# Kernel tuning notes

Measured on AMD Instinct MI355X. Metric: run time of the kernel, lower is better.

## Reference

```python
import jax, jax.numpy as jnp
import numpy as np

B, S, K, N, G = 4, 16, 8192, 8192, 128
NUM_GROUPS = K // G

def setup_inputs() -> dict:
    key = jax.random.key(0)
    k1, k2, k3, k4, k5 = jax.random.split(key, 5)
    x = jax.random.normal(k1, (B, S, K), dtype=jnp.float32)
    qweight = jax.random.randint(k2, (K, N), -128, 128, dtype=jnp.int32)
    # small positive scales like real quantizers produce
    scales = jax.random.uniform(k3, (NUM_GROUPS, N), dtype=jnp.float32) * 0.01 + 1e-4
    zeros = jax.random.uniform(k4, (NUM_GROUPS, N), dtype=jnp.float32) * 2.0 - 1.0
    bias = jax.random.normal(k5, (N,), dtype=jnp.float32)
    return {"x": x, "qweight": qweight, "scales": scales, "zeros": zeros,
            "bias": bias, "group_size": G}

def reference(x, qweight, scales, zeros, bias, group_size):
    # Expand per-group scale/zero along K: [num_groups, N] -> [K, N]
    Kdim = qweight.shape[0]
    if scales.shape[0] == 1:
        scale_exp = jnp.broadcast_to(scales, (Kdim, scales.shape[1]))
        zero_exp = jnp.broadcast_to(zeros, (Kdim, zeros.shape[1]))
    else:
        scale_exp = jnp.repeat(scales, group_size, axis=0)[:Kdim]
        zero_exp = jnp.repeat(zeros, group_size, axis=0)[:Kdim]
    # Dequantize: W[k, n] = (q - zero) * scale
    weight_fp = (qweight.astype(x.dtype) - zero_exp) * scale_exp  # [K, N]
    out = jnp.einsum('bsk,kn->bsn', x, weight_fp) + bias
    return out
```

## Files before the change

### kernel.cpp

```cpp
#include <hip/hip_runtime.h>

typedef __attribute__((ext_vector_type(8))) short short8;
typedef __attribute__((ext_vector_type(8))) unsigned short ushort8;
typedef __attribute__((ext_vector_type(4))) unsigned short ushort4v;
typedef __attribute__((ext_vector_type(4))) int int4v;
typedef __attribute__((ext_vector_type(4))) float f32x4;

#define Mdim 64
#define Kdim 8192
#define Ndim 8192
#define GRP 128
#define NGRP 64
#define KSPLIT 4
#define NG2 (NGRP / KSPLIT)
#define BN 128

#define SWZ(row, kk) ((row)*128 + ((kk) ^ (8*((((row) >> 3) ^ (row)) & 7))))

__device__ __forceinline__ unsigned short f2bf(float f) {
    unsigned int u = __builtin_bit_cast(unsigned int, f);
    u += 0x7FFFu + ((u >> 16) & 1u);
    return (unsigned short)(u >> 16);
}
__device__ __forceinline__ float bf2f(unsigned short h) {
    unsigned int u = ((unsigned int)h) << 16;
    return __builtin_bit_cast(float, u);
}

__global__ void prep_kernel(const float* __restrict__ x,
                            unsigned short* __restrict__ xh,
                            unsigned short* __restrict__ xl,
                            float* __restrict__ xsum) {
    const int tid = threadIdx.x;
    const int u = blockIdx.x * 8 + (tid >> 5);
    const int g = u & (NGRP - 1);
    const int m = u >> 6;
    const int lane = tid & 31;
    const int k = g * GRP + lane * 4;
    f32x4 v = *(const f32x4*)(x + (size_t)m * Kdim + k);
    ushort4v hv, lv;
    float s = 0.f;
#pragma unroll
    for (int i = 0; i < 4; ++i) {
        unsigned short h = f2bf(v[i]);
        hv[i] = h;
        lv[i] = f2bf(v[i] - bf2f(h));
        s += v[i];
    }
    *(ushort4v*)(xh + (size_t)m * Kdim + k) = hv;
    *(ushort4v*)(xl + (size_t)m * Kdim + k) = lv;
#pragma unroll
    for (int off = 16; off > 0; off >>= 1) s += __shfl_down(s, off, 32);
    if (lane == 0) xsum[g * Mdim + m] = s;
}

__global__ void init_kernel(const float* __restrict__ bias,
                            float* __restrict__ out) {
    const size_t e = ((size_t)blockIdx.x * 256 + threadIdx.x) * 4;
    const int n = (int)(e & (Ndim - 1));
    *(f32x4*)(out + e) = *(const f32x4*)(bias + n);
}

__launch_bounds__(512, 2)
__global__ void qlin_kernel(const unsigned short* __restrict__ xh,
                            const unsigned short* __restrict__ xl,
                            const int* __restrict__ qw,
                            const float* __restrict__ scales,
                            const float* __restrict__ zeros,
                            const float* __restrict__ xsum,
                            float* __restrict__ out) {
    __shared__ unsigned short lq[2][128 * 128];
    __shared__ unsigned short lxh[2][64 * 128];
    __shared__ unsigned short lxl[2][64 * 128];
    __shared__ float ls[NG2][128];
    __shared__ float lz[NG2][128];
    __shared__ float lxs[NG2][64];

    const int tid = threadIdx.x;
    const int kh = blockIdx.x & (KSPLIT - 1);
    const int n0 = (blockIdx.x >> 2) * BN;
    const int g0 = kh * NG2;

    const int w = tid >> 6;
    const int l = tid & 63;
    const int lcol = l & 15;
    const int lhi = l >> 4;
    const int mt = (w >> 2) * 32;
    const int ns = (w & 3) * 32;

    const int qc = tid & 31;
    const int qr = tid >> 5;
    const int xc = tid & 15;
    const int xm = tid >> 4;

    const int c0 = n0 + ns + lcol;
    const int c1 = c0 + 16;

    int4v qv[8];
    ushort8 xga, xgb, xgc, xgd;

    auto LOADX = [&](int g) {
        const size_t kb = (size_t)g * GRP + xc * 8;
        xga = *(const ushort8*)(xh + (size_t)xm * Kdim + kb);
        xgb = *(const ushort8*)(xh + (size_t)(xm + 32) * Kdim + kb);
        xgc = *(const ushort8*)(xl + (size_t)xm * Kdim + kb);
        xgd = *(const ushort8*)(xl + (size_t)(xm + 32) * Kdim + kb);
    };
    auto LOADQ = [&](int g) {
        const size_t kb = (size_t)g * GRP + qr * 8;
        const int nc = n0 + qc * 4;
#pragma unroll
        for (int j = 0; j < 8; ++j)
            qv[j] = *(const int4v*)(qw + (kb + j) * Ndim + nc);
    };
    auto WRITEX = [&](int b) {
        *(ushort8*)&lxh[b][SWZ(xm, xc * 8)] = xga;
        *(ushort8*)&lxh[b][SWZ(xm + 32, xc * 8)] = xgb;
        *(ushort8*)&lxl[b][SWZ(xm, xc * 8)] = xgc;
        *(ushort8*)&lxl[b][SWZ(xm + 32, xc * 8)] = xgd;
    };
    auto WRITEQ = [&](int b) {
#pragma unroll
        for (int i = 0; i < 4; ++i) {
            int4v pk;
#pragma unroll
            for (int t = 0; t < 4; ++t) {
                unsigned lo = __builtin_bit_cast(unsigned, (float)qv[2 * t][i]) >> 16;
                unsigned hi = __builtin_bit_cast(unsigned, (float)qv[2 * t + 1][i]) & 0xFFFF0000u;
                pk[t] = (int)(lo | hi);
            }
            *(int4v*)&lq[b][SWZ(qc * 4 + i, qr * 8)] = pk;
        }
    };

    f32x4 acc00 = {0,0,0,0}, acc01 = {0,0,0,0}, acc10 = {0,0,0,0}, acc11 = {0,0,0,0};

    {
        const int tg = tid >> 5, tc = tid & 31;
        f32x4 sv = *(const f32x4*)(scales + (size_t)(g0 + tg) * Ndim + n0 + tc * 4);
        f32x4 zv = *(const f32x4*)(zeros + (size_t)(g0 + tg) * Ndim + n0 + tc * 4);
        float x0 = xsum[(g0 + (tid >> 6)) * Mdim + (tid & 63)];
        float x1 = xsum[(g0 + ((tid + 512) >> 6)) * Mdim + (tid & 63)];
        LOADX(g0);
        LOADQ(g0);
        *(f32x4*)&ls[tg][tc * 4] = sv;
        *(f32x4*)&lz[tg][tc * 4] = zv;
        (&lxs[0][0])[tid] = x0;
        (&lxs[0][0])[tid + 512] = x1;
        WRITEX(0);
        WRITEQ(0);
        LOADX(g0 + 1);
        LOADQ(g0 + 1);
        asm volatile("s_waitcnt lgkmcnt(0)" ::: "memory");
        __builtin_amdgcn_s_barrier();
    }

    for (int g = 0; g < NG2; ++g) {
        const int b = g & 1;

        f32x4 p00 = {0,0,0,0}, p01 = {0,0,0,0}, p10 = {0,0,0,0}, p11 = {0,0,0,0};
#pragma unroll
        for (int ks = 0; ks < 4; ++ks) {
            const int kk = ks * 32 + lhi * 8;
            short8 bq0 = *(const short8*)&lq[b][SWZ(ns + lcol, kk)];
            short8 bq1 = *(const short8*)&lq[b][SWZ(ns + 16 + lcol, kk)];
            short8 ah0 = *(const short8*)&lxh[b][SWZ(mt + lcol, kk)];
            short8 al0 = *(const short8*)&lxl[b][SWZ(mt + lcol, kk)];
            short8 ah1 = *(const short8*)&lxh[b][SWZ(mt + 16 + lcol, kk)];
            short8 al1 = *(const short8*)&lxl[b][SWZ(mt + 16 + lcol, kk)];
            p00 = __builtin_amdgcn_mfma_f32_16x16x32_bf16(ah0, bq0, p00, 0, 0, 0);
            p00 = __builtin_amdgcn_mfma_f32_16x16x32_bf16(al0, bq0, p00, 0, 0, 0);
            p01 = __builtin_amdgcn_mfma_f32_16x16x32_bf16(ah0, bq1, p01, 0, 0, 0);
            p01 = __builtin_amdgcn_mfma_f32_16x16x32_bf16(al0, bq1, p01, 0, 0, 0);
            p10 = __builtin_amdgcn_mfma_f32_16x16x32_bf16(ah1, bq0, p10, 0, 0, 0);
            p10 = __builtin_amdgcn_mfma_f32_16x16x32_bf16(al1, bq0, p10, 0, 0, 0);
            p11 = __builtin_amdgcn_mfma_f32_16x16x32_bf16(ah1, bq1, p11, 0, 0, 0);
            p11 = __builtin_amdgcn_mfma_f32_16x16x32_bf16(al1, bq1, p11, 0, 0, 0);
        }
        {
            const float s0 = ls[g][ns + lcol],      z0 = lz[g][ns + lcol];
            const float s1 = ls[g][ns + 16 + lcol], z1 = lz[g][ns + 16 + lcol];
            f32x4 xs0 = *(const f32x4*)&lxs[g][mt + lhi * 4];
            f32x4 xs1 = *(const f32x4*)&lxs[g][mt + 16 + lhi * 4];
#pragma unroll
            for (int r = 0; r < 4; ++r) {
                acc00[r] += s0 * (p00[r] - z0 * xs0[r]);
                acc01[r] += s1 * (p01[r] - z1 * xs0[r]);
                acc10[r] += s0 * (p10[r] - z0 * xs1[r]);
                acc11[r] += s1 * (p11[r] - z1 * xs1[r]);
            }
        }

        if (g + 1 < NG2) {
            WRITEX(b ^ 1);
            if (g + 2 < NG2) {
                LOADX(g0 + g + 2);
                __builtin_amdgcn_sched_barrier(0);
            }
            WRITEQ(b ^ 1);
            if (g + 2 < NG2) {
                LOADQ(g0 + g + 2);
                __builtin_amdgcn_sched_barrier(0);
            }
            asm volatile("s_waitcnt lgkmcnt(0)" ::: "memory");
            __builtin_amdgcn_s_barrier();
        }
    }

#pragma unroll
    for (int r = 0; r < 4; ++r) {
        atomicAdd(out + (size_t)(mt + lhi * 4 + r) * Ndim + c0, acc00[r]);
        atomicAdd(out + (size_t)(mt + lhi * 4 + r) * Ndim + c1, acc01[r]);
        atomicAdd(out + (size_t)(mt + 16 + lhi * 4 + r) * Ndim + c0, acc10[r]);
        atomicAdd(out + (size_t)(mt + 16 + lhi * 4 + r) * Ndim + c1, acc11[r]);
    }
}

extern "C" void kernel_launch(void* const* d_in, const int* in_sizes, int n_in,
                              void* d_out, int out_size, void* d_ws, size_t ws_size,
                              hipStream_t stream) {
    const float* x = (const float*)d_in[0];
    const int* qw = (const int*)d_in[1];
    const float* scales = (const float*)d_in[2];
    const float* zeros = (const float*)d_in[3];
    const float* bias = (const float*)d_in[4];

    unsigned short* xh = (unsigned short*)d_ws;
    unsigned short* xl = xh + (size_t)Mdim * Kdim;
    float* xsum = (float*)(xl + (size_t)Mdim * Kdim);
    float* out = (float*)d_out;

    prep_kernel<<<512, 256, 0, stream>>>(x, xh, xl, xsum);
    init_kernel<<<(Mdim * Ndim / 4) / 256, 256, 0, stream>>>(bias, out);
    qlin_kernel<<<(Ndim / BN) * KSPLIT, 512, 0, stream>>>(xh, xl, qw, scales, zeros, xsum, out);
}
```

Before: 56.85 us.

## Single-buffer LDS, double K-split, fuse prep and bias init kernels

Drops LDS double buffering and the shared-memory copies of scales, zeros and xsum. These values are now prefetched into registers per group, and an extra barrier is added before LDS overwrite. With less LDS per block, launch bounds rise to 4 blocks per CU and KSPLIT doubles to 8, giving twice as many blocks. The prep and bias-init kernels are merged into one launch. The trade-offs are an extra barrier per group, less overlap between loads and compute, and twice as many atomic adds to the output.

```diff
diff --git a/kernel.cpp b/kernel.cpp
--- a/kernel.cpp
+++ b/kernel.cpp
@@ -11,7 +11,7 @@
 #define Ndim 8192
 #define GRP 128
 #define NGRP 64
-#define KSPLIT 4
+#define KSPLIT 8
 #define NG2 (NGRP / KSPLIT)
 #define BN 128
 
@@ -27,11 +27,19 @@
     return __builtin_bit_cast(float, u);
 }
 
-__global__ void prep_kernel(const float* __restrict__ x,
-                            unsigned short* __restrict__ xh,
-                            unsigned short* __restrict__ xl,
-                            float* __restrict__ xsum) {
+__global__ void prep_init_kernel(const float* __restrict__ x,
+                                 unsigned short* __restrict__ xh,
+                                 unsigned short* __restrict__ xl,
+                                 float* __restrict__ xsum,
+                                 const float* __restrict__ bias,
+                                 float* __restrict__ out) {
     const int tid = threadIdx.x;
+    if (blockIdx.x >= 512) {
+        const size_t e = ((size_t)(blockIdx.x - 512) * 256 + tid) * 4;
+        const int n = (int)(e & (Ndim - 1));
+        *(f32x4*)(out + e) = *(const f32x4*)(bias + n);
+        return;
+    }
     const int u = blockIdx.x * 8 + (tid >> 5);
     const int g = u & (NGRP - 1);
     const int m = u >> 6;
@@ -54,14 +62,7 @@
     if (lane == 0) xsum[g * Mdim + m] = s;
 }
 
-__global__ void init_kernel(const float* __restrict__ bias,
-                            float* __restrict__ out) {
-    const size_t e = ((size_t)blockIdx.x * 256 + threadIdx.x) * 4;
-    const int n = (int)(e & (Ndim - 1));
-    *(f32x4*)(out + e) = *(const f32x4*)(bias + n);
-}
-
-__launch_bounds__(512, 2)
+__launch_bounds__(512, 4)
 __global__ void qlin_kernel(const unsigned short* __restrict__ xh,
                             const unsigned short* __restrict__ xl,
                             const int* __restrict__ qw,
@@ -69,16 +70,13 @@
                             const float* __restrict__ zeros,
                             const float* __restrict__ xsum,
                             float* __restrict__ out) {
-    __shared__ unsigned short lq[2][128 * 128];
-    __shared__ unsigned short lxh[2][64 * 128];
-    __shared__ unsigned short lxl[2][64 * 128];
-    __shared__ float ls[NG2][128];
-    __shared__ float lz[NG2][128];
-    __shared__ float lxs[NG2][64];
+    __shared__ unsigned short lq[128 * 128];
+    __shared__ unsigned short lxh[64 * 128];
+    __shared__ unsigned short lxl[64 * 128];
 
     const int tid = threadIdx.x;
     const int kh = blockIdx.x & (KSPLIT - 1);
-    const int n0 = (blockIdx.x >> 2) * BN;
+    const int n0 = (blockIdx.x >> 3) * BN;
     const int g0 = kh * NG2;
 
     const int w = tid >> 6;
@@ -98,7 +96,17 @@
 
     int4v qv[8];
     ushort8 xga, xgb, xgc, xgd;
-
+    float sn0, sn1, zn0, zn1, sc0, sc1, zc0, zc1;
+    f32x4 xsn0, xsn1, xsc0, xsc1;
+
+    auto LOAD_SZX = [&](int g) {
+        sn0 = scales[(size_t)g * Ndim + c0];
+        sn1 = scales[(size_t)g * Ndim + c1];
+        zn0 = zeros[(size_t)g * Ndim + c0];
+        zn1 = zeros[(size_t)g * Ndim + c1];
+        xsn0 = *(const f32x4*)(xsum + g * Mdim + mt + lhi * 4);
+        xsn1 = *(const f32x4*)(xsum + g * Mdim + mt + 16 + lhi * 4);
+    };
     auto LOADX = [&](int g) {
         const size_t kb = (size_t)g * GRP + xc * 8;
         xga = *(const ushort8*)(xh + (size_t)xm * Kdim + kb);
@@ -113,13 +121,13 @@
         for (int j = 0; j < 8; ++j)
             qv[j] = *(const int4v*)(qw + (kb + j) * Ndim + nc);
     };
-    auto WRITEX = [&](int b) {
-        *(ushort8*)&lxh[b][SWZ(xm, xc * 8)] = xga;
-        *(ushort8*)&lxh[b][SWZ(xm + 32, xc * 8)] = xgb;
-        *(ushort8*)&lxl[b][SWZ(xm, xc * 8)] = xgc;
-        *(ushort8*)&lxl[b][SWZ(xm + 32, xc * 8)] = xgd;
-    };
-    auto WRITEQ = [&](int b) {
+    auto WRITEX = [&]() {
+        *(ushort8*)&lxh[SWZ(xm, xc * 8)] = xga;
+        *(ushort8*)&lxh[SWZ(xm + 32, xc * 8)] = xgb;
+        *(ushort8*)&lxl[SWZ(xm, xc * 8)] = xgc;
+        *(ushort8*)&lxl[SWZ(xm + 32, xc * 8)] = xgd;
+    };
+    auto WRITEQ = [&]() {
 #pragma unroll
         for (int i = 0; i < 4; ++i) {
             int4v pk;
@@ -129,45 +137,38 @@
                 unsigned hi = __builtin_bit_cast(unsigned, (float)qv[2 * t + 1][i]) & 0xFFFF0000u;
                 pk[t] = (int)(lo | hi);
             }
-            *(int4v*)&lq[b][SWZ(qc * 4 + i, qr * 8)] = pk;
-        }
+            *(int4v*)&lq[SWZ(qc * 4 + i, qr * 8)] = pk;
+        }
+    };
+    auto CCOPY = [&]() {
+        sc0 = sn0; sc1 = sn1; zc0 = zn0; zc1 = zn1; xsc0 = xsn0; xsc1 = xsn1;
     };
 
     f32x4 acc00 = {0,0,0,0}, acc01 = {0,0,0,0}, acc10 = {0,0,0,0}, acc11 = {0,0,0,0};
 
-    {
-        const int tg = tid >> 5, tc = tid & 31;
-        f32x4 sv = *(const f32x4*)(scales + (size_t)(g0 + tg) * Ndim + n0 + tc * 4);
-        f32x4 zv = *(const f32x4*)(zeros + (size_t)(g0 + tg) * Ndim + n0 + tc * 4);
-        float x0 = xsum[(g0 + (tid >> 6)) * Mdim + (tid & 63)];
-        float x1 = xsum[(g0 + ((tid + 512) >> 6)) * Mdim + (tid & 63)];
-        LOADX(g0);
-        LOADQ(g0);
-        *(f32x4*)&ls[tg][tc * 4] = sv;
-        *(f32x4*)&lz[tg][tc * 4] = zv;
-        (&lxs[0][0])[tid] = x0;
-        (&lxs[0][0])[tid + 512] = x1;
-        WRITEX(0);
-        WRITEQ(0);
-        LOADX(g0 + 1);
-        LOADQ(g0 + 1);
-        asm volatile("s_waitcnt lgkmcnt(0)" ::: "memory");
-        __builtin_amdgcn_s_barrier();
-    }
+    LOAD_SZX(g0);
+    LOADX(g0);
+    LOADQ(g0);
+    WRITEX();
+    WRITEQ();
+    CCOPY();
+    LOAD_SZX(g0 + 1);
+    LOADX(g0 + 1);
+    LOADQ(g0 + 1);
+    asm volatile("s_waitcnt lgkmcnt(0)" ::: "memory");
+    __builtin_amdgcn_s_barrier();
 
     for (int g = 0; g < NG2; ++g) {
-        const int b = g & 1;
-
         f32x4 p00 = {0,0,0,0}, p01 = {0,0,0,0}, p10 = {0,0,0,0}, p11 = {0,0,0,0};
 #pragma unroll
         for (int ks = 0; ks < 4; ++ks) {
             const int kk = ks * 32 + lhi * 8;
-            short8 bq0 = *(const short8*)&lq[b][SWZ(ns + lcol, kk)];
-            short8 bq1 = *(const short8*)&lq[b][SWZ(ns + 16 + lcol, kk)];
-            short8 ah0 = *(const short8*)&lxh[b][SWZ(mt + lcol, kk)];
-            short8 al0 = *(const short8*)&lxl[b][SWZ(mt + lcol, kk)];
-            short8 ah1 = *(const short8*)&lxh[b][SWZ(mt + 16 + lcol, kk)];
-            short8 al1 = *(const short8*)&lxl[b][SWZ(mt + 16 + lcol, kk)];
+            short8 bq0 = *(const short8*)&lq[SWZ(ns + lcol, kk)];
+            short8 bq1 = *(const short8*)&lq[SWZ(ns + 16 + lcol, kk)];
+            short8 ah0 = *(const short8*)&lxh[SWZ(mt + lcol, kk)];
+            short8 al0 = *(const short8*)&lxl[SWZ(mt + lcol, kk)];
+            short8 ah1 = *(const short8*)&lxh[SWZ(mt + 16 + lcol, kk)];
+            short8 al1 = *(const short8*)&lxl[SWZ(mt + 16 + lcol, kk)];
             p00 = __builtin_amdgcn_mfma_f32_16x16x32_bf16(ah0, bq0, p00, 0, 0, 0);
             p00 = __builtin_amdgcn_mfma_f32_16x16x32_bf16(al0, bq0, p00, 0, 0, 0);
             p01 = __builtin_amdgcn_mfma_f32_16x16x32_bf16(ah0, bq1, p01, 0, 0, 0);
@@ -177,27 +178,24 @@
             p11 = __builtin_amdgcn_mfma_f32_16x16x32_bf16(ah1, bq1, p11, 0, 0, 0);
             p11 = __builtin_amdgcn_mfma_f32_16x16x32_bf16(al1, bq1, p11, 0, 0, 0);
         }
-        {
-            const float s0 = ls[g][ns + lcol],      z0 = lz[g][ns + lcol];
-            const float s1 = ls[g][ns + 16 + lcol], z1 = lz[g][ns + 16 + lcol];
-            f32x4 xs0 = *(const f32x4*)&lxs[g][mt + lhi * 4];
-            f32x4 xs1 = *(const f32x4*)&lxs[g][mt + 16 + lhi * 4];
-#pragma unroll
-            for (int r = 0; r < 4; ++r) {
-                acc00[r] += s0 * (p00[r] - z0 * xs0[r]);
-                acc01[r] += s1 * (p01[r] - z1 * xs0[r]);
-                acc10[r] += s0 * (p10[r] - z0 * xs1[r]);
-                acc11[r] += s1 * (p11[r] - z1 * xs1[r]);
-            }
+#pragma unroll
+        for (int r = 0; r < 4; ++r) {
+            acc00[r] += sc0 * (p00[r] - zc0 * xsc0[r]);
+            acc01[r] += sc1 * (p01[r] - zc1 * xsc0[r]);
+            acc10[r] += sc0 * (p10[r] - zc0 * xsc1[r]);
+            acc11[r] += sc1 * (p11[r] - zc1 * xsc1[r]);
         }
 
         if (g + 1 < NG2) {
-            WRITEX(b ^ 1);
+            __builtin_amdgcn_s_barrier();
+            WRITEX();
+            CCOPY();
             if (g + 2 < NG2) {
+                LOAD_SZX(g0 + g + 2);
                 LOADX(g0 + g + 2);
                 __builtin_amdgcn_sched_barrier(0);
             }
-            WRITEQ(b ^ 1);
+            WRITEQ();
             if (g + 2 < NG2) {
                 LOADQ(g0 + g + 2);
                 __builtin_amdgcn_sched_barrier(0);
@@ -230,7 +228,6 @@
     float* xsum = (float*)(xl + (size_t)Mdim * Kdim);
     float* out = (float*)d_out;
 
-    prep_kernel<<<512, 256, 0, stream>>>(x, xh, xl, xsum);
-    init_kernel<<<(Mdim * Ndim / 4) / 256, 256, 0, stream>>>(bias, out);
+    prep_init_kernel<<<1024, 256, 0, stream>>>(x, xh, xl, xsum, bias, out);
     qlin_kernel<<<(Ndim / BN) * KSPLIT, 512, 0, stream>>>(xh, xl, qw, scales, zeros, xsum, out);
 }
```

Result: slower. 145.2 us (+155.4%).
